# Kernel optimization log

Hardware: AMD Instinct MI355X
Metric: run time of the kernel (lower is better)

## Reference

```python
import jax, jax.numpy as jnp
import numpy as np

WIDTH = 64  # attention_width
EPS = 1e-7  # K.epsilon()


def setup_inputs() -> dict:
    key = jax.random.key(0)
    k1, k2, k3, k4 = jax.random.split(key, 4)
    B, T, D, U = 4, 1024, 512, 32
    x = jax.random.normal(k1, (B, T, D), dtype=jnp.float32)
    Wt = jax.random.normal(k2, (D, U), dtype=jnp.float32) * (1.0 / np.sqrt(D))
    Wx = jax.random.normal(k3, (D, U), dtype=jnp.float32) * (1.0 / np.sqrt(D))
    bh = jnp.zeros((U,), dtype=jnp.float32)
    Wa = jax.random.normal(k4, (U, 1), dtype=jnp.float32) * (1.0 / np.sqrt(U))
    ba = jnp.zeros((1,), dtype=jnp.float32)
    return {"x": x, "Wt": Wt, "Wx": Wx, "bh": bh, "Wa": Wa, "ba": ba}


def reference(x, Wt, Wx, bh, Wa, ba):
    # x: [B, T, D]
    B, T, D = x.shape
    q = x @ Wt  # [B, T, U]
    k = x @ Wx  # [B, T, U]
    # additive emission: h[b,t,j,u] = tanh(q[b,t,u] + k[b,j,u] + bh[u])
    h = jnp.tanh(q[:, :, None, :] + k[:, None, :, :] + bh)  # [B, T, T, U]
    e = jnp.einsum('btju,u->btj', h, Wa[:, 0]) + ba[0]  # [B, T, T]
    e = jnp.exp(e)
    # banded local window: tf.matrix_band_part(ones, W//2, (W-1)//2)
    idx = jnp.arange(T)
    di = idx[:, None] - idx[None, :]  # i - j
    local = ((di <= WIDTH // 2) & (-di <= (WIDTH - 1) // 2)).astype(x.dtype)
    e = e * local[None, :, :]
    s = jnp.sum(e, axis=-1, keepdims=True)  # [B, T, 1]
    a = e / (s + EPS)  # attention weights [B, T, T]
    v = jnp.einsum('btj,bjd->btd', a, x)  # [B, T, D]
    return v
```

## Files before the change

kernel.cpp:

```cpp
#include <hip/hip_runtime.h>
#include <hip/hip_bf16.h>

#define B 4
#define T 1024
#define D 512
#define U 32
#define WIN 64
#define EPS 1e-7f

__device__ __forceinline__ float fast_tanh(float z) {
    const float ez = __expf(2.0f * z);
    return 1.0f - 2.0f / (ez + 1.0f);
}

__device__ __forceinline__ float bcast_lane(float v, int l) {
    return __int_as_float(__builtin_amdgcn_readlane(__float_as_int(v), l));
}

__global__ __launch_bounds__(512) void qk_kernel(
    const float* __restrict__ x, const float* __restrict__ Wt,
    const float* __restrict__ Wx, const float* __restrict__ bh,
    float* __restrict__ qk)
{
    __shared__ float W2[D][64];

    const int tid  = threadIdx.x;
    const int lane = tid & 63;
    const int wv   = tid >> 6;
    const int bid  = blockIdx.x;
    const int r0   = (bid & 7) * 512 + (bid >> 3) * 16 + wv * 2;

    {
        const float4* Wt4 = (const float4*)Wt;
        const float4* Wx4 = (const float4*)Wx;
        #pragma unroll
        for (int i = 0; i < 8; ++i) {
            const int j  = i * 512 + tid;
            const int d  = j >> 3;
            const int u0 = (j & 7) << 2;
            *(float4*)&W2[d][u0]      = Wt4[j];
            *(float4*)&W2[d][32 + u0] = Wx4[j];
        }
    }

    const float4* xr0 = (const float4*)(x + (size_t)(r0 + 0) * D);
    const float4* xr1 = (const float4*)(x + (size_t)(r0 + 1) * D);
    const float4 A0 = xr0[lane * 2], A1 = xr0[lane * 2 + 1];
    const float4 B0 = xr1[lane * 2], B1 = xr1[lane * 2 + 1];
    const float xa[8] = {A0.x, A0.y, A0.z, A0.w, A1.x, A1.y, A1.z, A1.w};
    const float xb[8] = {B0.x, B0.y, B0.z, B0.w, B1.x, B1.y, B1.z, B1.w};

    __syncthreads();

    const float bias = (lane < U) ? bh[lane] : 0.0f;
    float acc0 = bias, acc1 = bias;

    #pragma unroll
    for (int l = 0; l < 64; ++l) {
        #pragma unroll
        for (int r = 0; r < 8; ++r) {
            const float w  = W2[l * 8 + r][lane];
            const float s0 = bcast_lane(xa[r], l);
            const float s1 = bcast_lane(xb[r], l);
            acc0 = fmaf(s0, w, acc0);
            acc1 = fmaf(s1, w, acc1);
        }
    }

    qk[(size_t)(r0 + 0) * WIN + lane] = acc0;
    qk[(size_t)(r0 + 1) * WIN + lane] = acc1;
}

__global__ __launch_bounds__(256) void attn_kernel(
    const float* __restrict__ x, const float* __restrict__ qk,
    const float* __restrict__ Wa, const float* __restrict__ ba,
    float* __restrict__ out)
{
    __shared__ float A[2][4][64];

    const int tid  = threadIdx.x;
    const int lane = tid & 63;
    const int wv   = tid >> 6;
    const int l    = ((blockIdx.x & 7) << 6) + (blockIdx.x >> 3);
    const int qs   = wv >> 1;
    const int dh   = wv & 1;
    const int g0   = l * 8 + qs * 4;
    const int b    = g0 >> 10;
    const int t0   = g0 & (T - 1);

    #pragma unroll
    for (int i = 0; i < 2; ++i) {
        const int tt = t0 + dh * 2 + i;
        const float* qrow = qk + (size_t)(b * T + tt) * WIN;
        const int jj = tt - 32 + lane;
        float e = 0.0f;
        if (jj >= 0 && jj < T) {
            const float* krow = qk + (size_t)(b * T + jj) * WIN + U;
            float acc = ba[0];
            #pragma unroll
            for (int i4 = 0; i4 < 8; ++i4) {
                const float4 kv = ((const float4*)krow)[i4];
                const float4 qv = ((const float4*)qrow)[i4];
                acc = fmaf(Wa[i4 * 4 + 0], fast_tanh(qv.x + kv.x), acc);
                acc = fmaf(Wa[i4 * 4 + 1], fast_tanh(qv.y + kv.y), acc);
                acc = fmaf(Wa[i4 * 4 + 2], fast_tanh(qv.z + kv.z), acc);
                acc = fmaf(Wa[i4 * 4 + 3], fast_tanh(qv.w + kv.w), acc);
            }
            e = __expf(acc);
        }
        float s = e;
        #pragma unroll
        for (int off = 32; off > 0; off >>= 1)
            s += __shfl_xor(s, off);
        A[qs][dh * 2 + i][lane] = e / (s + EPS);
    }
    __syncthreads();

    const float w0 = A[qs][0][lane];
    const float w1 = A[qs][1][lane];
    const float w2 = A[qs][2][lane];
    const float w3 = A[qs][3][lane];

    float4 v0 = make_float4(0.f,0.f,0.f,0.f), v1 = v0, v2 = v0, v3 = v0;
    const float* xh = x + (size_t)b * T * D + dh * (D / 2);

    #pragma unroll
    for (int m = 0; m < 67; ++m) {
        int row = t0 - 32 + m;
        row = (row < 0) ? 0 : row;
        row = (row > T - 1) ? (T - 1) : row;
        const float4 xv = ((const float4*)(xh + (size_t)row * D))[lane];
        if (m <= 63) {
            const float a0 = bcast_lane(w0, m);
            v0.x = fmaf(a0, xv.x, v0.x); v0.y = fmaf(a0, xv.y, v0.y);
            v0.z = fmaf(a0, xv.z, v0.z); v0.w = fmaf(a0, xv.w, v0.w);
        }
        if (m >= 1 && m <= 64) {
            const float a1 = bcast_lane(w1, m - 1);
            v1.x = fmaf(a1, xv.x, v1.x); v1.y = fmaf(a1, xv.y, v1.y);
            v1.z = fmaf(a1, xv.z, v1.z); v1.w = fmaf(a1, xv.w, v1.w);
        }
        if (m >= 2 && m <= 65) {
            const float a2 = bcast_lane(w2, m - 2);
            v2.x = fmaf(a2, xv.x, v2.x); v2.y = fmaf(a2, xv.y, v2.y);
            v2.z = fmaf(a2, xv.z, v2.z); v2.w = fmaf(a2, xv.w, v2.w);
        }
        if (m >= 3) {
            const float a3 = bcast_lane(w3, m - 3);
            v3.x = fmaf(a3, xv.x, v3.x); v3.y = fmaf(a3, xv.y, v3.y);
            v3.z = fmaf(a3, xv.z, v3.z); v3.w = fmaf(a3, xv.w, v3.w);
        }
    }

    float* ob = out + (size_t)(b * T + t0) * D + dh * (D / 2);
    ((float4*)(ob + 0 * D))[lane] = v0;
    ((float4*)(ob + 1 * D))[lane] = v1;
    ((float4*)(ob + 2 * D))[lane] = v2;
    ((float4*)(ob + 3 * D))[lane] = v3;
}

extern "C" void kernel_launch(void* const* d_in, const int* in_sizes, int n_in,
                              void* d_out, int out_size, void* d_ws, size_t ws_size,
                              hipStream_t stream)
{
    const float* x  = (const float*)d_in[0];
    const float* Wt = (const float*)d_in[1];
    const float* Wx = (const float*)d_in[2];
    const float* bh = (const float*)d_in[3];
    const float* Wa = (const float*)d_in[4];
    const float* ba = (const float*)d_in[5];
    float* out = (float*)d_out;
    float* qk  = (float*)d_ws;

    qk_kernel<<<dim3(256), dim3(512), 0, stream>>>(x, Wt, Wx, bh, qk);
    attn_kernel<<<dim3(512), dim3(256), 0, stream>>>(x, qk, Wa, ba, out);
}
```

Baseline: 93.19 us.

## Stage shared x window in LDS per block of 32 queries

The attention kernel now gives each block 32 query rows and one half of D. It loads the 96-row x window into shared memory once, and every wave reads its 67 rows from LDS instead of from global memory. Attention weights stay in registers per wave instead of going through shared memory. This cuts redundant global loads of overlapping x rows. In exchange it uses 96 KB of LDS per block, which limits occupancy, and the grid shrinks to 256 blocks.

Result: slower. 99.24 us (+6.5%).

```diff
diff --git a/kernel.cpp b/kernel.cpp
--- a/kernel.cpp
+++ b/kernel.cpp
@@ -71,26 +71,44 @@
     qk[(size_t)(r0 + 1) * WIN + lane] = acc1;
 }
 
-__global__ __launch_bounds__(256) void attn_kernel(
+__global__ __launch_bounds__(512) void attn_kernel(
     const float* __restrict__ x, const float* __restrict__ qk,
     const float* __restrict__ Wa, const float* __restrict__ ba,
     float* __restrict__ out)
 {
-    __shared__ float A[2][4][64];
+    __shared__ float xs[96 * 256];
 
     const int tid  = threadIdx.x;
     const int lane = tid & 63;
-    const int wv   = tid >> 6;
-    const int l    = ((blockIdx.x & 7) << 6) + (blockIdx.x >> 3);
-    const int qs   = wv >> 1;
-    const int dh   = wv & 1;
-    const int g0   = l * 8 + qs * 4;
+    const int wq   = tid >> 6;
+    const int bid  = blockIdx.x;
+    const int c    = bid & 7;
+    const int rr   = bid >> 3;
+    const int g    = c * 16 + (rr >> 1);
+    const int dh   = rr & 1;
+    const int g0   = g * 32;
     const int b    = g0 >> 10;
     const int t0   = g0 & (T - 1);
+    const int tq   = t0 + wq * 4;
+
+    const float* xh = x + (size_t)b * T * D + dh * (D / 2);
 
     #pragma unroll
-    for (int i = 0; i < 2; ++i) {
-        const int tt = t0 + dh * 2 + i;
+    for (int i = 0; i < 12; ++i) {
+        const int idx = i * 512 + tid;
+        const int lr  = idx >> 6;
+        const int c4  = idx & 63;
+        int grow = t0 - 32 + lr;
+        grow = (grow < 0) ? 0 : grow;
+        grow = (grow > T - 1) ? (T - 1) : grow;
+        *(float4*)&xs[lr * 256 + c4 * 4] =
+            *(const float4*)(xh + (size_t)grow * D + c4 * 4);
+    }
+
+    float wgt[4];
+    #pragma unroll
+    for (int i = 0; i < 4; ++i) {
+        const int tt = tq + i;
         const float* qrow = qk + (size_t)(b * T + tt) * WIN;
         const int jj = tt - 32 + lane;
         float e = 0.0f;
@@ -112,47 +130,39 @@
         #pragma unroll
         for (int off = 32; off > 0; off >>= 1)
             s += __shfl_xor(s, off);
-        A[qs][dh * 2 + i][lane] = e / (s + EPS);
+        wgt[i] = e / (s + EPS);
     }
     __syncthreads();
 
-    const float w0 = A[qs][0][lane];
-    const float w1 = A[qs][1][lane];
-    const float w2 = A[qs][2][lane];
-    const float w3 = A[qs][3][lane];
-
     float4 v0 = make_float4(0.f,0.f,0.f,0.f), v1 = v0, v2 = v0, v3 = v0;
-    const float* xh = x + (size_t)b * T * D + dh * (D / 2);
+    const float* xw = &xs[(size_t)wq * 4 * 256];
 
     #pragma unroll
     for (int m = 0; m < 67; ++m) {
-        int row = t0 - 32 + m;
-        row = (row < 0) ? 0 : row;
-        row = (row > T - 1) ? (T - 1) : row;
-        const float4 xv = ((const float4*)(xh + (size_t)row * D))[lane];
+        const float4 xv = *(const float4*)&xw[m * 256 + lane * 4];
         if (m <= 63) {
-            const float a0 = bcast_lane(w0, m);
+            const float a0 = bcast_lane(wgt[0], m);
             v0.x = fmaf(a0, xv.x, v0.x); v0.y = fmaf(a0, xv.y, v0.y);
             v0.z = fmaf(a0, xv.z, v0.z); v0.w = fmaf(a0, xv.w, v0.w);
         }
         if (m >= 1 && m <= 64) {
-            const float a1 = bcast_lane(w1, m - 1);
+            const float a1 = bcast_lane(wgt[1], m - 1);
             v1.x = fmaf(a1, xv.x, v1.x); v1.y = fmaf(a1, xv.y, v1.y);
             v1.z = fmaf(a1, xv.z, v1.z); v1.w = fmaf(a1, xv.w, v1.w);
         }
         if (m >= 2 && m <= 65) {
-            const float a2 = bcast_lane(w2, m - 2);
+            const float a2 = bcast_lane(wgt[2], m - 2);
             v2.x = fmaf(a2, xv.x, v2.x); v2.y = fmaf(a2, xv.y, v2.y);
             v2.z = fmaf(a2, xv.z, v2.z); v2.w = fmaf(a2, xv.w, v2.w);
         }
         if (m >= 3) {
-            const float a3 = bcast_lane(w3, m - 3);
+            const float a3 = bcast_lane(wgt[3], m - 3);
             v3.x = fmaf(a3, xv.x, v3.x); v3.y = fmaf(a3, xv.y, v3.y);
             v3.z = fmaf(a3, xv.z, v3.z); v3.w = fmaf(a3, xv.w, v3.w);
         }
     }
 
-    float* ob = out + (size_t)(b * T + t0) * D + dh * (D / 2);
+    float* ob = out + (size_t)(b * T + tq) * D + dh * (D / 2);
     ((float4*)(ob + 0 * D))[lane] = v0;
     ((float4*)(ob + 1 * D))[lane] = v1;
     ((float4*)(ob + 2 * D))[lane] = v2;
@@ -173,5 +183,5 @@
     float* qk  = (float*)d_ws;
 
     qk_kernel<<<dim3(256), dim3(512), 0, stream>>>(x, Wt, Wx, bh, qk);
-    attn_kernel<<<dim3(512), dim3(256), 0, stream>>>(x, qk, Wa, ba, out);
+    attn_kernel<<<dim3(256), dim3(512), 0, stream>>>(x, qk, Wa, ba, out);
 }
```
